# Performance work log

Hardware: AMD Instinct MI355X
Metric: run time of the kernel (lower is better)

## Reference

```python
import jax, jax.numpy as jnp
import numpy as np

B, S, V, D, H, DK, DFF, L = 2, 1024, 513, 512, 8, 64, 2048, 6
PAD_IDX = -1.0
EPS_GPE = 0.1

def _sinusoid_table(n_position, d_hid):
    pos = np.arange(n_position)[:, None].astype(np.float64)
    i = np.arange(d_hid)[None, :]
    angle = pos / np.power(10000.0, 2 * (i // 2) / d_hid)
    tab = np.zeros((n_position, d_hid), dtype=np.float32)
    tab[:, 0::2] = np.sin(angle[:, 0::2])
    tab[:, 1::2] = np.cos(angle[:, 1::2])
    return jnp.asarray(tab)

_POS_TABLE = _sinusoid_table(2048, D)

def _ln(x, g, b, eps=1e-6):
    m = x.mean(-1, keepdims=True)
    v = x.var(-1, keepdims=True)
    return (x - m) * jax.lax.rsqrt(v + eps) * g + b

def _mha(x_q, x_kv, wq_, wk_, wv_, wo_, mask, g, b):
    Bq, Sq, _ = x_q.shape
    Skv = x_kv.shape[1]
    q = (x_q @ wq_).reshape(Bq, Sq, H, DK).transpose(0, 2, 1, 3)
    k = (x_kv @ wk_).reshape(Bq, Skv, H, DK).transpose(0, 2, 1, 3)
    v = (x_kv @ wv_).reshape(Bq, Skv, H, DK).transpose(0, 2, 1, 3)
    scores = jnp.einsum('bhqd,bhkd->bhqk', q, k) / np.float32(np.sqrt(DK))
    scores = jnp.where(mask[:, None], scores, jnp.float32(-1e9))
    attn = jax.nn.softmax(scores, axis=-1)
    out = jnp.einsum('bhqk,bhkd->bhqd', attn, v).transpose(0, 2, 1, 3).reshape(Bq, Sq, D)
    return _ln(x_q + out @ wo_, g, b)

def _forward(dec_in, prev_dec_out, trg, adj, graph_length, gr_mask, gr_pos_enc_kernel,
             emb_w1, emb_b1, emb_w2, emb_b2, emb_w3, emb_b3, ln0_g, ln0_b,
             wq, wk, wv, wo, ln1_g, ln1_b,
             cq, ck, cv, co, ln2_g, ln2_b,
             ffn_w1, ffn_b1, ffn_w2, ffn_b2, ln3_g, ln3_b,
             p_w1, p_b1, p_w2, p_b2, p_w3, p_b3):
    # masks (n_ensemble = 1 so dec_in[:, :, 0, :] == dec_in)
    causal = jnp.tril(jnp.ones((S, S), bool))
    slf_mask = jnp.all(dec_in != PAD_IDX, -1)[:, None, :] & causal          # [B,S,S]
    enc_mask = jnp.all(prev_dec_out != PAD_IDX, -1)[:, None, :]             # [B,1,S]
    # word-embedding MLP: 513 -> 513 -> 513 -> 512
    h = jax.nn.relu(dec_in @ emb_w1 + emb_b1)
    h = jax.nn.relu(h @ emb_w2 + emb_b2)
    h = h @ emb_w3 + emb_b3                                                 # [B,S,D]
    # propagation graph positional encoding (k = 0..2, un-normalized branch)
    w = (1.0 - EPS_GPE) ** jnp.arange(gr_pos_enc_kernel.shape[1], dtype=jnp.float32)
    base = _POS_TABLE[:S]                                                   # [S,D]
    emb = jnp.einsum('k,bkst,td->bsd', w, gr_pos_enc_kernel, base) / w.sum()
    h = _ln(h + emb, ln0_g, ln0_b)
    for i in range(L):
        h = _mha(h, h, wq[i], wk[i], wv[i], wo[i], slf_mask, ln1_g[i], ln1_b[i])
        h = _mha(h, prev_dec_out, cq[i], ck[i], cv[i], co[i], enc_mask, ln2_g[i], ln2_b[i])
        f = jax.nn.relu(h @ ffn_w1[i] + ffn_b1[i]) @ ffn_w2[i] + ffn_b2[i]
        h = _ln(h + f, ln3_g[i], ln3_b[i])
    # projection head: 512 -> 513 -> 513 -> 513
    z = jax.nn.relu(h @ p_w1 + p_b1)
    z = jax.nn.relu(z @ p_w2 + p_b2)
    return z @ p_w3 + p_b3                                                  # [B,S,V]

def setup_inputs():
    key = jax.random.key(0)
    ks = jax.random.split(key, 24)
    def xavier(k, shape):
        lim = np.float32(np.sqrt(6.0 / (shape[-2] + shape[-1])))
        return jax.random.uniform(k, shape, jnp.float32, -lim, lim)
    inp = {}
    inp['dec_in'] = jax.random.uniform(ks[0], (B, S, V), jnp.float32)
    inp['prev_dec_out'] = jax.random.normal(ks[1], (B, S, D), jnp.float32)
    inp['trg'] = jnp.zeros((B, S, V), jnp.float32)
    inp['adj'] = jnp.zeros((B, S, S), jnp.float32)
    inp['graph_length'] = jnp.zeros((B, S, 10), jnp.float32)
    inp['gr_mask'] = jnp.zeros((B, 1, S, S), jnp.float32)
    gk = jax.random.uniform(ks[2], (B, 3, S, S), jnp.float32)
    inp['gr_pos_enc_kernel'] = gk / jnp.sum(gk, -1, keepdims=True)  # row-stochastic diffusion kernels
    SZ = max(V, D)  # sz_intermed = 513
    inp['emb_w1'] = xavier(ks[3], (V, SZ)); inp['emb_b1'] = jnp.zeros((SZ,))
    inp['emb_w2'] = xavier(ks[4], (SZ, SZ)); inp['emb_b2'] = jnp.zeros((SZ,))
    inp['emb_w3'] = xavier(ks[5], (SZ, D)); inp['emb_b3'] = jnp.zeros((D,))
    inp['ln0_g'] = jnp.ones((D,)); inp['ln0_b'] = jnp.zeros((D,))
    for name, ki, shp in [('wq', 6, (L, D, D)), ('wk', 7, (L, D, D)), ('wv', 8, (L, D, D)), ('wo', 9, (L, D, D)),
                          ('cq', 10, (L, D, D)), ('ck', 11, (L, D, D)), ('cv', 12, (L, D, D)), ('co', 13, (L, D, D)),
                          ('ffn_w1', 14, (L, D, DFF)), ('ffn_w2', 15, (L, DFF, D))]:
        inp[name] = xavier(ks[ki], shp)
    inp['ffn_b1'] = jnp.zeros((L, DFF)); inp['ffn_b2'] = jnp.zeros((L, D))
    inp['ln1_g'] = jnp.ones((L, D)); inp['ln1_b'] = jnp.zeros((L, D))
    inp['ln2_g'] = jnp.ones((L, D)); inp['ln2_b'] = jnp.zeros((L, D))
    inp['ln3_g'] = jnp.ones((L, D)); inp['ln3_b'] = jnp.zeros((L, D))
    inp['p_w1'] = xavier(ks[16], (D, V)); inp['p_b1'] = jnp.zeros((V,))
    inp['p_w2'] = xavier(ks[17], (V, V)); inp['p_b2'] = jnp.zeros((V,))
    inp['p_w3'] = xavier(ks[18], (V, V)); inp['p_b3'] = jnp.zeros((V,))
    return inp

def reference(dec_in, prev_dec_out, trg, adj, graph_length, gr_mask, gr_pos_enc_kernel,
              emb_w1, emb_b1, emb_w2, emb_b2, emb_w3, emb_b3, ln0_g, ln0_b,
              wq, wk, wv, wo, ln1_g, ln1_b,
              cq, ck, cv, co, ln2_g, ln2_b,
              ffn_w1, ffn_b1, ffn_w2, ffn_b2, ln3_g, ln3_b,
              p_w1, p_b1, p_w2, p_b2, p_w3, p_b3):
    return _forward(dec_in, prev_dec_out, trg, adj, graph_length, gr_mask, gr_pos_enc_kernel,
                    emb_w1, emb_b1, emb_w2, emb_b2, emb_w3, emb_b3, ln0_g, ln0_b,
                    wq, wk, wv, wo, ln1_g, ln1_b,
                    cq, ck, cv, co, ln2_g, ln2_b,
                    ffn_w1, ffn_b1, ffn_w2, ffn_b2, ln3_g, ln3_b,
                    p_w1, p_b1, p_w2, p_b2, p_w3, p_b3)
```

## Files before the change

kernel.cpp:

```cpp
#include <hip/hip_runtime.h>
#include <hip/hip_bf16.h>
#include <stdint.h>

#define BB 2
#define SS 1024
#define VV 513
#define VP 576
#define DD 512
#define HH 8
#define DKK 64
#define DFFN 2048
#define LL 6
#define MM (BB * SS)

typedef __bf16 bf16x8 __attribute__((ext_vector_type(8)));
typedef float f32x4 __attribute__((ext_vector_type(4)));
typedef unsigned short us8 __attribute__((ext_vector_type(8)));
typedef unsigned short us4 __attribute__((ext_vector_type(4)));

static __device__ inline unsigned short f2bf(float f) {
  union { float f; unsigned u; } v; v.f = f;
  unsigned u = v.u;
  unsigned r = (u + 0x7FFFu + ((u >> 16) & 1u)) >> 16;
  return (unsigned short)r;
}

static __device__ inline bf16x8 ldfrag(const unsigned short* p) {
  us8 r = *(const us8*)p;
  return __builtin_bit_cast(bf16x8, r);
}

typedef __attribute__((address_space(3))) void lds_void;
typedef const __attribute__((address_space(1))) void glb_void;
static __device__ inline void gl_lds16(const void* g, void* l) {
  __builtin_amdgcn_global_load_lds((glb_void*)g, (lds_void*)l, 16, 0, 0);
}

static __device__ inline bf16x8 ldfrag_swz(const unsigned short* base, int row, int kloc) {
  const unsigned byte = (unsigned)(row * 128 + kloc * 2) ^ (unsigned)((row & 7) << 4);
  return ldfrag((const unsigned short*)((const char*)base + byte));
}

static __device__ inline int rot3(int x) { return (x == 2) ? 0 : x + 1; }

struct GemmP {
  const unsigned short* A;
  const unsigned short* B0; const unsigned short* B1; const unsigned short* B2;
  const float* bias;
  float* C;
  unsigned short* D0; unsigned short* D1; unsigned short* D2;
  int Kp, Np, ldc, Nreal, relu;
};

template<int NB, int NT, int TRV, int KS>
__global__ __launch_bounds__(256)
void gemm_tpl(GemmP p)
{
  constexpr int FN = NT / 32;
  __shared__ unsigned short Al[3][64 * 64];
  __shared__ unsigned short Bl[3][NT * 64];
  const int tid = threadIdx.x;
  const int l = tid & 63, w = tid >> 6;
  const int wm = w >> 1, wn = w & 1;
  const int lr = l & 15, lg = l >> 4;

  const int nbn = p.Np / NT;
  int sel = 0, bx = blockIdx.x;
  if (NB > 1) { sel = bx / nbn; bx -= sel * nbn; }
  const unsigned short* Bmat = p.B0;
  if (NB > 1 && sel == 1) Bmat = p.B1;
  if (NB > 2 && sel == 2) Bmat = p.B2;
  const int m0 = blockIdx.y << 6, n0 = bx * NT;
  const int kz = (KS > 1) ? blockIdx.z : 0;

  f32x4 acc[2][FN];
  const f32x4 zf = {0.f, 0.f, 0.f, 0.f};
#pragma unroll
  for (int i = 0; i < 2; ++i)
#pragma unroll
    for (int j = 0; j < FN; ++j) acc[i][j] = zf;

  const size_t Kp = (size_t)p.Kp;
  const unsigned short* Abase = p.A + (size_t)m0 * Kp;
  const unsigned short* Bbase = Bmat + (size_t)n0 * Kp;
  const int nt = (p.Kp >> 6) / KS;
  const int kb0 = kz * nt;

  auto stage = [&](int buf, int kt) {
    const int k0 = (kb0 + kt) << 6;
#pragma unroll
    for (int j = 0; j < 2; ++j) {
      const int ti = j * 256 + tid;
      const int row = ti >> 3;
      const int ch = (ti & 7) ^ (row & 7);
      gl_lds16(Abase + (size_t)row * Kp + k0 + ch * 8, &Al[buf][ti * 8]);
    }
#pragma unroll
    for (int j = 0; j < FN; ++j) {
      const int ti = j * 256 + tid;
      const int row = ti >> 3;
      const int ch = (ti & 7) ^ (row & 7);
      gl_lds16(Bbase + (size_t)row * Kp + k0 + ch * 8, &Bl[buf][ti * 8]);
    }
  };

  stage(0, 0);
  if (nt > 1) stage(1, 1);
  int cb = 0, sb = 2;

  for (int kt = 0; kt < nt; ++kt) {
    if (kt + 1 < nt) {
      if constexpr (FN == 2) asm volatile("s_waitcnt vmcnt(4)" ::: "memory");
      else                   asm volatile("s_waitcnt vmcnt(6)" ::: "memory");
    } else {
      asm volatile("s_waitcnt vmcnt(0)" ::: "memory");
    }
    __builtin_amdgcn_s_barrier();
    if (kt + 2 < nt) { stage(sb, kt + 2); sb = rot3(sb); }
#pragma unroll
    for (int ks = 0; ks < 2; ++ks) {
      bf16x8 af[2], bfv[FN];
#pragma unroll
      for (int mf = 0; mf < 2; ++mf)
        af[mf] = ldfrag_swz(Al[cb], wm * 32 + mf * 16 + lr, ks * 32 + lg * 8);
#pragma unroll
      for (int nf = 0; nf < FN; ++nf)
        bfv[nf] = ldfrag_swz(Bl[cb], wn * (NT / 2) + nf * 16 + lr, ks * 32 + lg * 8);
#pragma unroll
      for (int mf = 0; mf < 2; ++mf)
#pragma unroll
        for (int nf = 0; nf < FN; ++nf)
          acc[mf][nf] = __builtin_amdgcn_mfma_f32_16x16x32_bf16(af[mf], bfv[nf], acc[mf][nf], 0, 0, 0);
    }
    cb = rot3(cb);
  }

  unsigned short* Dsel = p.D0;
  if (NB > 1 && sel == 1) Dsel = p.D1;
  if (NB > 2 && sel == 2) Dsel = p.D2;

  if (TRV && sel == 2) {
#pragma unroll
    for (int mf = 0; mf < 2; ++mf) {
      const int growb = m0 + wm * 32 + mf * 16 + (lg << 2);
      const int b = growb >> 10, s = growb & 1023;
#pragma unroll
      for (int nf = 0; nf < FN; ++nf) {
        const int gcol = n0 + wn * (NT / 2) + nf * 16 + lr;
        const int h = gcol >> 6, d = gcol & 63;
        us4 t;
#pragma unroll
        for (int r = 0; r < 4; ++r) t[r] = f2bf(acc[mf][nf][r]);
        *(us4*)(Dsel + (((size_t)(b * HH) + h) * DKK + d) * SS + s) = t;
      }
    }
    return;
  }

  float* Cz = p.C ? (p.C + (size_t)kz * MM * p.ldc) : nullptr;
#pragma unroll
  for (int mf = 0; mf < 2; ++mf) {
#pragma unroll
    for (int r = 0; r < 4; ++r) {
      const int grow = m0 + wm * 32 + mf * 16 + (lg << 2) + r;
#pragma unroll
      for (int nf = 0; nf < FN; ++nf) {
        const int gcol = n0 + wn * (NT / 2) + nf * 16 + lr;
        float v = acc[mf][nf][r];
        if (p.bias && kz == 0 && gcol < p.Nreal) v += p.bias[gcol];
        if (p.relu) v = fmaxf(v, 0.f);
        if (Dsel) Dsel[(size_t)grow * p.Np + gcol] = f2bf(v);
        if (Cz && gcol < p.Nreal) Cz[(size_t)grow * p.ldc + gcol] = v;
      }
    }
  }
}

struct GemmBat {
  const unsigned short* A;
  const unsigned short* B[12];
  unsigned short* D[12];
  int Kp, Np;
};

__global__ __launch_bounds__(256)
void gemm_bat(GemmBat p)
{
  __shared__ unsigned short Al[3][64 * 64];
  __shared__ unsigned short Bl[3][64 * 64];
  const int tid = threadIdx.x;
  const int l = tid & 63, w = tid >> 6;
  const int wm = w >> 1, wn = w & 1;
  const int lr = l & 15, lg = l >> 4;

  const int nbn = p.Np >> 6;
  const int sel = blockIdx.x / nbn;
  const int bx = blockIdx.x - sel * nbn;
  const unsigned short* Bmat = p.B[sel];
  unsigned short* Dmat = p.D[sel];
  const int m0 = blockIdx.y << 6, n0 = bx << 6;

  f32x4 acc[2][2];
  const f32x4 zf = {0.f, 0.f, 0.f, 0.f};
#pragma unroll
  for (int i = 0; i < 2; ++i)
#pragma unroll
    for (int j = 0; j < 2; ++j) acc[i][j] = zf;

  const size_t Kp = (size_t)p.Kp;
  const unsigned short* Abase = p.A + (size_t)m0 * Kp;
  const unsigned short* Bbase = Bmat + (size_t)n0 * Kp;

  auto stage = [&](int buf, int kt) {
    const int k0 = kt << 6;
#pragma unroll
    for (int j = 0; j < 2; ++j) {
      const int ti = j * 256 + tid;
      const int row = ti >> 3;
      const int ch = (ti & 7) ^ (row & 7);
      gl_lds16(Abase + (size_t)row * Kp + k0 + ch * 8, &Al[buf][ti * 8]);
    }
#pragma unroll
    for (int j = 0; j < 2; ++j) {
      const int ti = j * 256 + tid;
      const int row = ti >> 3;
      const int ch = (ti & 7) ^ (row & 7);
      gl_lds16(Bbase + (size_t)row * Kp + k0 + ch * 8, &Bl[buf][ti * 8]);
    }
  };

  const int nt = p.Kp >> 6;
  stage(0, 0);
  if (nt > 1) stage(1, 1);
  int cb = 0, sb = 2;

  for (int kt = 0; kt < nt; ++kt) {
    if (kt + 1 < nt) asm volatile("s_waitcnt vmcnt(4)" ::: "memory");
    else             asm volatile("s_waitcnt vmcnt(0)" ::: "memory");
    __builtin_amdgcn_s_barrier();
    if (kt + 2 < nt) { stage(sb, kt + 2); sb = rot3(sb); }
#pragma unroll
    for (int ks = 0; ks < 2; ++ks) {
      bf16x8 af[2], bfv[2];
#pragma unroll
      for (int mf = 0; mf < 2; ++mf)
        af[mf] = ldfrag_swz(Al[cb], wm * 32 + mf * 16 + lr, ks * 32 + lg * 8);
#pragma unroll
      for (int nf = 0; nf < 2; ++nf)
        bfv[nf] = ldfrag_swz(Bl[cb], wn * 32 + nf * 16 + lr, ks * 32 + lg * 8);
#pragma unroll
      for (int mf = 0; mf < 2; ++mf)
#pragma unroll
        for (int nf = 0; nf < 2; ++nf)
          acc[mf][nf] = __builtin_amdgcn_mfma_f32_16x16x32_bf16(af[mf], bfv[nf], acc[mf][nf], 0, 0, 0);
    }
    cb = rot3(cb);
  }

  if (sel & 1) {
#pragma unroll
    for (int mf = 0; mf < 2; ++mf) {
      const int growb = m0 + wm * 32 + mf * 16 + (lg << 2);
      const int b = growb >> 10, s = growb & 1023;
#pragma unroll
      for (int nf = 0; nf < 2; ++nf) {
        const int gcol = n0 + wn * 32 + nf * 16 + lr;
        const int h = gcol >> 6, d = gcol & 63;
        us4 t;
#pragma unroll
        for (int r = 0; r < 4; ++r) t[r] = f2bf(acc[mf][nf][r]);
        *(us4*)(Dmat + (((size_t)(b * HH) + h) * DKK + d) * SS + s) = t;
      }
    }
    return;
  }

#pragma unroll
  for (int mf = 0; mf < 2; ++mf) {
#pragma unroll
    for (int r = 0; r < 4; ++r) {
      const int grow = m0 + wm * 32 + mf * 16 + (lg << 2) + r;
#pragma unroll
      for (int nf = 0; nf < 2; ++nf) {
        const int gcol = n0 + wn * 32 + nf * 16 + lr;
        Dmat[(size_t)grow * p.Np + gcol] = f2bf(acc[mf][nf][r]);
      }
    }
  }
}

template<int CAUSAL>
__global__ __launch_bounds__(128)
void attn_kernel(const unsigned short* __restrict__ Qb,
                 const unsigned short* __restrict__ Kb,
                 const unsigned short* __restrict__ VbT,
                 unsigned short* __restrict__ Ob,
                 const float* __restrict__ maskadd)
{
  __shared__ unsigned short Kl[2][2][64 * 64];
  __shared__ unsigned short Vl[2][2][64 * 64];
  __shared__ char PC[9216];
  unsigned short* Pl = (unsigned short*)PC;
  float (*comb)[66] = (float(*)[66])PC;

  const int tid = threadIdx.x;
  const int l = tid & 63, w = tid >> 6;
  const int qt = blockIdx.x, h = blockIdx.y, b = blockIdx.z;
  const int lr = l & 15, lg = l >> 4;

  bf16x8 qf[2][2];
#pragma unroll
  for (int mf = 0; mf < 2; ++mf) {
    const unsigned short* qrow = Qb + ((size_t)(b * SS) + qt * 32 + mf * 16 + lr) * DD + h * DKK;
    qf[mf][0] = ldfrag(qrow + (lg << 3));
    qf[mf][1] = ldfrag(qrow + 32 + (lg << 3));
  }

  const unsigned short* Kbase = Kb + (size_t)(b * SS) * DD + h * DKK;
  const unsigned short* Vbase = VbT + ((size_t)(b * HH) + h) * DKK * SS;

  auto stage = [&](int buf, int kt) {
#pragma unroll
    for (int j = 0; j < 8; ++j) {
      const int ti = j * 64 + l;
      const int row = ti >> 3;
      const int ch = (ti & 7) ^ (row & 7);
      gl_lds16(Kbase + (size_t)(kt * 64 + row) * DD + ch * 8, &Kl[w][buf][ti * 8]);
    }
#pragma unroll
    for (int j = 0; j < 8; ++j) {
      const int ti = j * 64 + l;
      const int row = ti >> 3;
      const int ch = (ti & 7) ^ (row & 7);
      gl_lds16(Vbase + (size_t)row * SS + kt * 64 + ch * 8, &Vl[w][buf][ti * 8]);
    }
  };

  f32x4 accO[2][4];
  const f32x4 zf = {0.f, 0.f, 0.f, 0.f};
#pragma unroll
  for (int mf = 0; mf < 2; ++mf)
#pragma unroll
    for (int nf = 0; nf < 4; ++nf) accO[mf][nf] = zf;
  float mold[2][4], lsum[2][4];
#pragma unroll
  for (int mf = 0; mf < 2; ++mf)
#pragma unroll
    for (int r = 0; r < 4; ++r) { mold[mf][r] = -1e30f; lsum[mf][r] = 0.f; }

  const int ktmax = CAUSAL ? ((qt >> 1) + 1) : (SS / 64);
  const int myn = (ktmax - w + 1) >> 1;

  if (myn > 0) stage(0, w);
  int buf = 0;

  for (int i = 0; i < myn; ++i) {
    const int kt = w + 2 * i;
    if (i + 1 < myn) {
      stage(buf ^ 1, kt + 2);
      asm volatile("s_waitcnt vmcnt(16)" ::: "memory");
    } else {
      asm volatile("s_waitcnt vmcnt(0)" ::: "memory");
    }
    const unsigned short* KB = &Kl[w][buf][0];
    const unsigned short* VB = &Vl[w][buf][0];
    float sc[2][4][4];
    __builtin_amdgcn_s_setprio(1);
#pragma unroll
    for (int nf = 0; nf < 4; ++nf) {
      bf16x8 k0 = ldfrag_swz(KB, nf * 16 + lr, lg * 8);
      bf16x8 k1 = ldfrag_swz(KB, nf * 16 + lr, 32 + lg * 8);
      const int kglob = kt * 64 + nf * 16 + lr;
      const float madd = maskadd[b * SS + kglob];
#pragma unroll
      for (int mf = 0; mf < 2; ++mf) {
        f32x4 s = zf;
        s = __builtin_amdgcn_mfma_f32_16x16x32_bf16(qf[mf][0], k0, s, 0, 0, 0);
        s = __builtin_amdgcn_mfma_f32_16x16x32_bf16(qf[mf][1], k1, s, 0, 0, 0);
#pragma unroll
        for (int r = 0; r < 4; ++r) {
          const int qglob = qt * 32 + mf * 16 + (lg << 2) + r;
          sc[mf][nf][r] = (CAUSAL && kglob > qglob) ? -1e9f : s[r] * 0.125f + madd;
        }
      }
    }
    __builtin_amdgcn_s_setprio(0);
#pragma unroll
    for (int mf = 0; mf < 2; ++mf)
#pragma unroll
      for (int r = 0; r < 4; ++r) {
        float mloc = fmaxf(fmaxf(sc[mf][0][r], sc[mf][1][r]), fmaxf(sc[mf][2][r], sc[mf][3][r]));
#pragma unroll
        for (int off = 1; off < 16; off <<= 1)
          mloc = fmaxf(mloc, __shfl_xor(mloc, off, 64));
        const float mnew = fmaxf(mold[mf][r], mloc);
        const float corr = __expf(mold[mf][r] - mnew);
        float ps = 0.f;
#pragma unroll
        for (int nf = 0; nf < 4; ++nf) {
          const float pv = __expf(sc[mf][nf][r] - mnew);
          sc[mf][nf][r] = pv;
          ps += pv;
        }
#pragma unroll
        for (int off = 1; off < 16; off <<= 1)
          ps += __shfl_xor(ps, off, 64);
        lsum[mf][r] = lsum[mf][r] * corr + ps;
#pragma unroll
        for (int nf = 0; nf < 4; ++nf) accO[mf][nf][r] *= corr;
        mold[mf][r] = mnew;
      }
    unsigned short* pw = Pl + w * 32 * 72;
#pragma unroll
    for (int mf = 0; mf < 2; ++mf)
#pragma unroll
      for (int nf = 0; nf < 4; ++nf)
#pragma unroll
        for (int r = 0; r < 4; ++r)
          pw[(mf * 16 + (lg << 2) + r) * 72 + nf * 16 + lr] = f2bf(sc[mf][nf][r]);
    bf16x8 pa[2][2];
#pragma unroll
    for (int mf = 0; mf < 2; ++mf) {
      pa[mf][0] = ldfrag(&pw[(mf * 16 + lr) * 72 + (lg << 3)]);
      pa[mf][1] = ldfrag(&pw[(mf * 16 + lr) * 72 + 32 + (lg << 3)]);
    }
    __builtin_amdgcn_s_setprio(1);
#pragma unroll
    for (int nf = 0; nf < 4; ++nf) {
      bf16x8 v0 = ldfrag_swz(VB, nf * 16 + lr, lg * 8);
      bf16x8 v1 = ldfrag_swz(VB, nf * 16 + lr, 32 + lg * 8);
#pragma unroll
      for (int mf = 0; mf < 2; ++mf) {
        accO[mf][nf] = __builtin_amdgcn_mfma_f32_16x16x32_bf16(pa[mf][0], v0, accO[mf][nf], 0, 0, 0);
        accO[mf][nf] = __builtin_amdgcn_mfma_f32_16x16x32_bf16(pa[mf][1], v1, accO[mf][nf], 0, 0, 0);
      }
    }
    __builtin_amdgcn_s_setprio(0);
    buf ^= 1;
  }

  __syncthreads();
  if (w == 1) {
#pragma unroll
    for (int mf = 0; mf < 2; ++mf)
#pragma unroll
      for (int r = 0; r < 4; ++r) {
        const int qrow = mf * 16 + (lg << 2) + r;
#pragma unroll
        for (int nf = 0; nf < 4; ++nf)
          comb[qrow][nf * 16 + lr] = accO[mf][nf][r];
        if (lr == 0) { comb[qrow][64] = mold[mf][r]; comb[qrow][65] = lsum[mf][r]; }
      }
  }
  __syncthreads();
  if (w == 0) {
#pragma unroll
    for (int mf = 0; mf < 2; ++mf)
#pragma unroll
      for (int r = 0; r < 4; ++r) {
        const int qrow = mf * 16 + (lg << 2) + r;
        const float m1 = comb[qrow][64], l1 = comb[qrow][65];
        const float m0v = mold[mf][r], l0 = lsum[mf][r];
        const float ms = fmaxf(m0v, m1);
        const float f0 = __expf(m0v - ms), f1 = __expf(m1 - ms);
        const float inv = 1.f / (l0 * f0 + l1 * f1);
        const size_t orow = ((size_t)(b * SS) + qt * 32 + mf * 16 + (lg << 2) + r) * DD + h * DKK;
#pragma unroll
        for (int nf = 0; nf < 4; ++nf)
          Ob[orow + nf * 16 + lr] =
              f2bf((accO[mf][nf][r] * f0 + comb[qrow][nf * 16 + lr] * f1) * inv);
      }
  }
}

template<int P>
__global__ __launch_bounds__(256)
void addln_kernel(const float* __restrict__ a, const float* __restrict__ c,
                  const float* __restrict__ g, const float* __restrict__ bb,
                  float* __restrict__ hf, unsigned short* __restrict__ hb)
{
  const int row = blockIdx.x * 4 + (threadIdx.x >> 6);
  const int l = threadIdx.x & 63;
  const float* ar = a + (size_t)row * DD + l * 8;
  f32x4 x0 = *(const f32x4*)ar;
  f32x4 x1 = *(const f32x4*)(ar + 4);
#pragma unroll
  for (int pp = 0; pp < P; ++pp) {
    const float* cr = c + (size_t)pp * MM * DD + (size_t)row * DD + l * 8;
    x0 += *(const f32x4*)cr;
    x1 += *(const f32x4*)(cr + 4);
  }
  float sum = x0[0] + x0[1] + x0[2] + x0[3] + x1[0] + x1[1] + x1[2] + x1[3];
#pragma unroll
  for (int off = 1; off < 64; off <<= 1) sum += __shfl_xor(sum, off, 64);
  const float mean = sum * (1.f / 512.f);
  float vs = 0.f;
#pragma unroll
  for (int j = 0; j < 4; ++j) { float d0 = x0[j] - mean; float d1 = x1[j] - mean; vs += d0 * d0 + d1 * d1; }
#pragma unroll
  for (int off = 1; off < 64; off <<= 1) vs += __shfl_xor(vs, off, 64);
  const float rs = rsqrtf(vs * (1.f / 512.f) + 1e-6f);
  const f32x4 g0 = *(const f32x4*)(g + l * 8), g1 = *(const f32x4*)(g + l * 8 + 4);
  const f32x4 b0 = *(const f32x4*)(bb + l * 8), b1 = *(const f32x4*)(bb + l * 8 + 4);
  f32x4 o0, o1;
  us8 ob;
#pragma unroll
  for (int j = 0; j < 4; ++j) {
    o0[j] = (x0[j] - mean) * rs * g0[j] + b0[j];
    o1[j] = (x1[j] - mean) * rs * g1[j] + b1[j];
    ob[j] = f2bf(o0[j]); ob[j + 4] = f2bf(o1[j]);
  }
  float* of = hf + (size_t)row * DD + l * 8;
  *(f32x4*)of = o0; *(f32x4*)(of + 4) = o1;
  *(us8*)(hb + (size_t)row * DD + l * 8) = ob;
}

template<int NCOLS, int NPAD>
__global__ __launch_bounds__(64)
void prep_row(const float* __restrict__ x, unsigned short* __restrict__ xb,
              float* __restrict__ mask)
{
  const int row = blockIdx.x, l = threadIdx.x;
  const float* xr = x + (size_t)row * NCOLS;
  unsigned short* ob = xb + (size_t)row * NPAD;
  int ok = 1;
  for (int j = l; j < NPAD; j += 64) {
    if (j < NCOLS) {
      const float v = xr[j];
      ok &= (v != -1.0f) ? 1 : 0;
      ob[j] = f2bf(v);
    } else {
      ob[j] = 0;
    }
  }
  ok = __all(ok) ? 1 : 0;
  if (l == 0) mask[row] = ok ? 0.f : -1e9f;
}

__global__ void postable_kernel(unsigned short* __restrict__ tabT)
{
  const int i = blockIdx.x * blockDim.x + threadIdx.x;
  if (i >= DD * SS) return;
  const int d = i >> 10, s = i & 1023;
  const float ex = (float)(2 * (d >> 1)) * (1.0f / (float)DD);
  const float ang = (float)s * exp2f(ex * -13.287712379549449f);
  tabT[i] = f2bf((d & 1) ? cosf(ang) : sinf(ang));
}

__global__ void gpec_kernel(const float* __restrict__ gk, unsigned short* __restrict__ Mb)
{
  const int i = blockIdx.x * blockDim.x + threadIdx.x;
  if (i >= BB * SS * SS) return;
  const int b = i / (SS * SS);
  const int rem = i - b * (SS * SS);
  const float* p = gk + (size_t)b * 3 * SS * SS + rem;
  Mb[i] = f2bf((p[0] + 0.9f * p[SS * SS] + 0.81f * p[2 * SS * SS]) * (1.0f / 2.71f));
}

__global__ __launch_bounds__(256)
void wconv_kernel(const float* __restrict__ W, unsigned short* __restrict__ WT,
                  int K, int N, int Kp, int Np)
{
  __shared__ float t[64][65];
  const float* Wl = W + (size_t)blockIdx.z * K * N;
  unsigned short* WTl = WT + (size_t)blockIdx.z * Np * Kp;
  const int n0 = blockIdx.x << 6, k0 = blockIdx.y << 6;
  const int tid = threadIdx.x;
  const int cx = tid & 63, ry = tid >> 6;
#pragma unroll
  for (int i = 0; i < 16; ++i) {
    const int kk = k0 + ry + i * 4, nn = n0 + cx;
    t[ry + i * 4][cx] = (kk < K && nn < N) ? Wl[(size_t)kk * N + nn] : 0.f;
  }
  __syncthreads();
#pragma unroll
  for (int i = 0; i < 16; ++i) {
    const int nn = n0 + ry + i * 4, kk = k0 + cx;
    WTl[(size_t)nn * Kp + kk] = f2bf(t[cx][ry + i * 4]);
  }
}

struct WconvB { const float* W[8]; unsigned short* WT[8]; };
__global__ __launch_bounds__(256)
void wconv8_kernel(WconvB p)
{
  __shared__ float t[64][65];
  const int z = blockIdx.z;
  const int wi = z / LL, li = z - wi * LL;
  const float* Wl = p.W[wi] + (size_t)li * DD * DD;
  unsigned short* WTl = p.WT[wi] + (size_t)li * DD * DD;
  const int n0 = blockIdx.x << 6, k0 = blockIdx.y << 6;
  const int cx = threadIdx.x & 63, ry = threadIdx.x >> 6;
#pragma unroll
  for (int i = 0; i < 16; ++i)
    t[ry + i * 4][cx] = Wl[(size_t)(k0 + ry + i * 4) * DD + n0 + cx];
  __syncthreads();
#pragma unroll
  for (int i = 0; i < 16; ++i)
    WTl[(size_t)(n0 + ry + i * 4) * DD + k0 + cx] = f2bf(t[cx][ry + i * 4]);
}

static inline void g1(hipStream_t s, const unsigned short* A, const unsigned short* B,
                      const float* bias, float* C, unsigned short* D,
                      int Kp, int Np, int ldc, int Nreal, int relu)
{
  GemmP p{};
  p.A = A; p.B0 = B; p.bias = bias; p.C = C; p.D0 = D;
  p.Kp = Kp; p.Np = Np; p.ldc = ldc; p.Nreal = Nreal; p.relu = relu;
  gemm_tpl<1, 64, 0, 1><<<dim3(Np >> 6, MM >> 6), 256, 0, s>>>(p);
}

static inline void g1w(hipStream_t s, const unsigned short* A, const unsigned short* B,
                       const float* bias, unsigned short* D, int Kp, int Np, int relu)
{
  GemmP p{};
  p.A = A; p.B0 = B; p.bias = bias; p.D0 = D;
  p.Kp = Kp; p.Np = Np; p.ldc = Np; p.Nreal = Np; p.relu = relu;
  gemm_tpl<1, 128, 0, 1><<<dim3(Np >> 7, MM >> 6), 256, 0, s>>>(p);
}

static inline void g1k4(hipStream_t s, const unsigned short* A, const unsigned short* B,
                        const float* bias, float* C, int Kp)
{
  GemmP p{};
  p.A = A; p.B0 = B; p.bias = bias; p.C = C;
  p.Kp = Kp; p.Np = DD; p.ldc = DD; p.Nreal = DD; p.relu = 0;
  gemm_tpl<1, 64, 0, 4><<<dim3(DD >> 6, MM >> 6, 4), 256, 0, s>>>(p);
}

static inline void g3t(hipStream_t s, const unsigned short* A, const unsigned short* B0,
                       const unsigned short* B1, const unsigned short* B2,
                       unsigned short* D0, unsigned short* D1, unsigned short* D2T)
{
  GemmP p{};
  p.A = A; p.B0 = B0; p.B1 = B1; p.B2 = B2; p.D0 = D0; p.D1 = D1; p.D2 = D2T;
  p.Kp = DD; p.Np = DD; p.ldc = DD; p.Nreal = DD; p.relu = 0;
  gemm_tpl<3, 64, 1, 1><<<dim3(3 * (DD >> 6), MM >> 6), 256, 0, s>>>(p);
}

extern "C" void kernel_launch(void* const* d_in, const int* in_sizes, int n_in,
                              void* d_out, int out_size, void* d_ws, size_t ws_size,
                              hipStream_t stream)
{
  (void)in_sizes; (void)n_in; (void)out_size; (void)ws_size;
  const float* dec_in = (const float*)d_in[0];
  const float* prev   = (const float*)d_in[1];
  const float* gk     = (const float*)d_in[6];
  const float* emb_w1 = (const float*)d_in[7];
  const float* emb_b1 = (const float*)d_in[8];
  const float* emb_w2 = (const float*)d_in[9];
  const float* emb_b2 = (const float*)d_in[10];
  const float* emb_w3 = (const float*)d_in[11];
  const float* emb_b3 = (const float*)d_in[12];
  const float* ln0_g  = (const float*)d_in[13];
  const float* ln0_b  = (const float*)d_in[14];
  const float* wq     = (const float*)d_in[15];
  const float* wk     = (const float*)d_in[16];
  const float* wv     = (const float*)d_in[17];
  const float* wo     = (const float*)d_in[18];
  const float* cq     = (const float*)d_in[19];
  const float* ck     = (const float*)d_in[20];
  const float* cv     = (const float*)d_in[21];
  const float* co     = (const float*)d_in[22];
  const float* ffn_w1 = (const float*)d_in[23];
  const float* ffn_w2 = (const float*)d_in[24];
  const float* ffn_b1 = (const float*)d_in[25];
  const float* ffn_b2 = (const float*)d_in[26];
  const float* ln1_g  = (const float*)d_in[27];
  const float* ln1_b  = (const float*)d_in[28];
  const float* ln2_g  = (const float*)d_in[29];
  const float* ln2_b  = (const float*)d_in[30];
  const float* ln3_g  = (const float*)d_in[31];
  const float* ln3_b  = (const float*)d_in[32];
  const float* p_w1   = (const float*)d_in[33];
  const float* p_b1   = (const float*)d_in[34];
  const float* p_w2   = (const float*)d_in[35];
  const float* p_b2   = (const float*)d_in[36];
  const float* p_w3   = (const float*)d_in[37];
  const float* p_b3   = (const float*)d_in[38];

  char* wsp = (char*)d_ws;
  auto carve = [&](size_t bytes) { char* r = wsp; wsp += (bytes + 255) & ~(size_t)255; return r; };

  unsigned short* decb  = (unsigned short*)carve((size_t)MM * VP * 2);
  unsigned short* prevb = (unsigned short*)carve((size_t)MM * DD * 2);
  float*          hf    = (float*)carve((size_t)MM * DD * 4);
  unsigned short* hb    = (unsigned short*)carve((size_t)MM * DD * 2);
  float*          xf1   = (float*)carve((size_t)MM * DD * 4);
  unsigned short* tb1   = (unsigned short*)carve((size_t)MM * DFFN * 2);
  unsigned short* Mbb   = tb1;
  float*          xf2   = (float*)((char*)tb1 + (size_t)MM * SS * 2);
  unsigned short* tb2a  = (unsigned short*)carve((size_t)MM * VP * 2);
  unsigned short* tb2b  = (unsigned short*)carve((size_t)MM * VP * 2);
  unsigned short* qb    = (unsigned short*)carve((size_t)MM * DD * 2);
  unsigned short* kb    = (unsigned short*)carve((size_t)MM * DD * 2);
  unsigned short* vbT   = (unsigned short*)carve((size_t)MM * DD * 2);
  float* kvs = (float*)carve((size_t)MM * 4);
  float* kve = (float*)carve((size_t)MM * 4);
  unsigned short* postabt = (unsigned short*)carve((size_t)DD * SS * 2);
  unsigned short* ew1t  = (unsigned short*)carve((size_t)VP * VP * 2);
  unsigned short* ew2t  = (unsigned short*)carve((size_t)VP * VP * 2);
  unsigned short* ew3t  = (unsigned short*)carve((size_t)DD * VP * 2);
  unsigned short* wqt   = (unsigned short*)carve((size_t)LL * DD * DD * 2);
  unsigned short* wkt   = (unsigned short*)carve((size_t)LL * DD * DD * 2);
  unsigned short* wvt   = (unsigned short*)carve((size_t)LL * DD * DD * 2);
  unsigned short* wot   = (unsigned short*)carve((size_t)LL * DD * DD * 2);
  unsigned short* cqt   = (unsigned short*)carve((size_t)LL * DD * DD * 2);
  unsigned short* ckt   = (unsigned short*)carve((size_t)LL * DD * DD * 2);
  unsigned short* cvt   = (unsigned short*)carve((size_t)LL * DD * DD * 2);
  unsigned short* cot   = (unsigned short*)carve((size_t)LL * DD * DD * 2);
  unsigned short* f1t   = (unsigned short*)carve((size_t)LL * DFFN * DD * 2);
  unsigned short* f2t   = (unsigned short*)carve((size_t)LL * DD * DFFN * 2);
  unsigned short* p1t   = (unsigned short*)carve((size_t)VP * DD * 2);
  unsigned short* p2t   = (unsigned short*)carve((size_t)VP * VP * 2);
  unsigned short* p3t   = (unsigned short*)carve((size_t)VP * VP * 2);
  unsigned short* ckall = (unsigned short*)carve((size_t)LL * MM * DD * 2);
  unsigned short* cvbT  = (unsigned short*)carve((size_t)LL * MM * DD * 2);
  float*          xk4   = (float*)carve((size_t)4 * MM * DD * 4);

  const dim3 agrid(SS / 32, HH, BB);

  prep_row<VV, VP><<<MM, 64, 0, stream>>>(dec_in, decb, kvs);
  prep_row<DD, DD><<<MM, 64, 0, stream>>>(prev, prevb, kve);
  postable_kernel<<<(DD * SS + 255) / 256, 256, 0, stream>>>(postabt);
  gpec_kernel<<<(BB * SS * SS + 255) / 256, 256, 0, stream>>>(gk, Mbb);

  {
    WconvB wb{};
    wb.W[0] = wq; wb.W[1] = wk; wb.W[2] = wv; wb.W[3] = wo;
    wb.W[4] = cq; wb.W[5] = ck; wb.W[6] = cv; wb.W[7] = co;
    wb.WT[0] = wqt; wb.WT[1] = wkt; wb.WT[2] = wvt; wb.WT[3] = wot;
    wb.WT[4] = cqt; wb.WT[5] = ckt; wb.WT[6] = cvt; wb.WT[7] = cot;
    wconv8_kernel<<<dim3(8, 8, 8 * LL), 256, 0, stream>>>(wb);
  }
  wconv_kernel<<<dim3(9, 9, 1), 256, 0, stream>>>(emb_w1, ew1t, VV, VV, VP, VP);
  wconv_kernel<<<dim3(9, 9, 1), 256, 0, stream>>>(emb_w2, ew2t, VV, VV, VP, VP);
  wconv_kernel<<<dim3(8, 9, 1), 256, 0, stream>>>(emb_w3, ew3t, VV, DD, VP, DD);
  wconv_kernel<<<dim3(32, 8, LL), 256, 0, stream>>>(ffn_w1, f1t, DD, DFFN, DD, DFFN);
  wconv_kernel<<<dim3(8, 32, LL), 256, 0, stream>>>(ffn_w2, f2t, DFFN, DD, DFFN, DD);
  wconv_kernel<<<dim3(9, 8, 1), 256, 0, stream>>>(p_w1, p1t, DD, VV, DD, VP);
  wconv_kernel<<<dim3(9, 9, 1), 256, 0, stream>>>(p_w2, p2t, VV, VV, VP, VP);
  wconv_kernel<<<dim3(9, 9, 1), 256, 0, stream>>>(p_w3, p3t, VV, VV, VP, VP);

  {
    GemmBat p{};
    p.A = prevb; p.Kp = DD; p.Np = DD;
    for (int i = 0; i < LL; ++i) {
      p.B[2 * i]     = ckt + (size_t)i * DD * DD;
      p.B[2 * i + 1] = cvt + (size_t)i * DD * DD;
      p.D[2 * i]     = ckall + (size_t)i * MM * DD;
      p.D[2 * i + 1] = cvbT + (size_t)i * MM * DD;
    }
    gemm_bat<<<dim3(12 * (DD >> 6), MM >> 6), 256, 0, stream>>>(p);
  }

  g1(stream, decb, ew1t, emb_b1, nullptr, tb2a, VP, VP, VP, VV, 1);
  g1(stream, tb2a, ew2t, emb_b2, nullptr, tb2b, VP, VP, VP, VV, 1);
  g1(stream, tb2b, ew3t, emb_b3, xf1, nullptr, VP, DD, DD, DD, 0);
  g1(stream, Mbb, postabt, nullptr, xf2, nullptr, SS, DD, DD, DD, 0);
  addln_kernel<1><<<MM / 4, 256, 0, stream>>>(xf1, xf2, ln0_g, ln0_b, hf, hb);

  for (int i = 0; i < LL; ++i) {
    const size_t od = (size_t)i * DD * DD;
    g3t(stream, hb, wqt + od, wkt + od, wvt + od, qb, kb, vbT);
    attn_kernel<1><<<agrid, 128, 0, stream>>>(qb, kb, vbT, qb, kvs);
    g1(stream, qb, wot + od, nullptr, xf1, nullptr, DD, DD, DD, DD, 0);
    addln_kernel<1><<<MM / 4, 256, 0, stream>>>(hf, xf1, ln1_g + i * DD, ln1_b + i * DD, hf, hb);
    g1(stream, hb, cqt + od, nullptr, nullptr, qb, DD, DD, DD, DD, 0);
    attn_kernel<0><<<agrid, 128, 0, stream>>>(qb, ckall + (size_t)i * MM * DD,
                                              cvbT + (size_t)i * MM * DD, qb, kve);
    g1(stream, qb, cot + od, nullptr, xf1, nullptr, DD, DD, DD, DD, 0);
    addln_kernel<1><<<MM / 4, 256, 0, stream>>>(hf, xf1, ln2_g + i * DD, ln2_b + i * DD, hf, hb);
    g1w(stream, hb, f1t + (size_t)i * DFFN * DD, ffn_b1 + i * DFFN, tb1, DD, DFFN, 1);
    g1k4(stream, tb1, f2t + (size_t)i * DD * DFFN, ffn_b2 + i * DD, xk4, DFFN);
    addln_kernel<4><<<MM / 4, 256, 0, stream>>>(hf, xk4, ln3_g + i * DD, ln3_b + i * DD, hf, hb);
  }

  g1(stream, hb, p1t, p_b1, nullptr, tb2a, DD, VP, VP, VV, 1);
  g1(stream, tb2a, p2t, p_b2, nullptr, tb2b, VP, VP, VP, VV, 1);
  g1(stream, tb2b, p3t, p_b3, (float*)d_out, nullptr, VP, VP, VV, VV, 0);
}
```

Baseline: 1.071 ms.

## Fuse cross-attention Q projection into attention kernel and merge setup kernels

Adds an attnx kernel that computes the cross-attention query projection (hb × cq slice per head) in-block before running flash attention over the encoder keys. This removes the separate Q GEMM launch and the round trip of Q through global memory. The output projections now use a 2-way split-K GEMM whose partial sums are reduced inside addln. The startup prep kernels are merged into one launch, and the weight conversion kernels into another, to cut launch overhead. The price is redundant Q-projection work, since each head block re-reads the hb rows, plus extra partial-sum traffic in addln.

```diff
diff --git a/kernel.cpp b/kernel.cpp
--- a/kernel.cpp
+++ b/kernel.cpp
@@ -289,7 +289,6 @@
   }
 }
 
-template<int CAUSAL>
 __global__ __launch_bounds__(128)
 void attn_kernel(const unsigned short* __restrict__ Qb,
                  const unsigned short* __restrict__ Kb,
@@ -348,7 +347,7 @@
 #pragma unroll
     for (int r = 0; r < 4; ++r) { mold[mf][r] = -1e30f; lsum[mf][r] = 0.f; }
 
-  const int ktmax = CAUSAL ? ((qt >> 1) + 1) : (SS / 64);
+  const int ktmax = (qt >> 1) + 1;
   const int myn = (ktmax - w + 1) >> 1;
 
   if (myn > 0) stage(0, w);
@@ -380,7 +379,7 @@
 #pragma unroll
         for (int r = 0; r < 4; ++r) {
           const int qglob = qt * 32 + mf * 16 + (lg << 2) + r;
-          sc[mf][nf][r] = (CAUSAL && kglob > qglob) ? -1e9f : s[r] * 0.125f + madd;
+          sc[mf][nf][r] = (kglob > qglob) ? -1e9f : s[r] * 0.125f + madd;
         }
       }
     }
@@ -473,6 +472,253 @@
   }
 }
 
+__global__ __launch_bounds__(128)
+void attnx_kernel(const unsigned short* __restrict__ Hb,
+                  const unsigned short* __restrict__ Wq,
+                  const unsigned short* __restrict__ Kb,
+                  const unsigned short* __restrict__ VbT,
+                  unsigned short* __restrict__ Ob,
+                  const float* __restrict__ maskadd)
+{
+  __shared__ unsigned short Kl[2][2][64 * 64];
+  __shared__ unsigned short Vl[2][2][64 * 64];
+  __shared__ char PC[9216];
+  unsigned short* Pl = (unsigned short*)PC;
+  float (*comb)[66] = (float(*)[66])PC;
+  unsigned short* QA = &Kl[0][0][0];
+  unsigned short* QB = &Vl[0][0][0];
+  unsigned short* Ql = (unsigned short*)PC;
+
+  const int tid = threadIdx.x;
+  const int l = tid & 63, w = tid >> 6;
+  const int qt = blockIdx.x, h = blockIdx.y, b = blockIdx.z;
+  const int lr = l & 15, lg = l >> 4;
+
+  {
+    const unsigned short* Abase = Hb + ((size_t)(b * SS) + qt * 32) * DD;
+    const unsigned short* Bbase = Wq + (size_t)(h * DKK) * DD;
+    auto stage_q = [&](int buf, int kt) {
+      const int k0 = kt << 6;
+#pragma unroll
+      for (int j = 0; j < 2; ++j) {
+        const int ti = j * 128 + tid;
+        const int row = ti >> 3;
+        const int ch = (ti & 7) ^ (row & 7);
+        gl_lds16(Abase + (size_t)row * DD + k0 + ch * 8, &QA[buf * 2048 + ti * 8]);
+      }
+#pragma unroll
+      for (int j = 0; j < 4; ++j) {
+        const int ti = j * 128 + tid;
+        const int row = ti >> 3;
+        const int ch = (ti & 7) ^ (row & 7);
+        gl_lds16(Bbase + (size_t)row * DD + k0 + ch * 8, &QB[buf * 4096 + ti * 8]);
+      }
+    };
+    f32x4 qacc[2][2];
+    const f32x4 zf = {0.f, 0.f, 0.f, 0.f};
+#pragma unroll
+    for (int i = 0; i < 2; ++i)
+#pragma unroll
+      for (int j = 0; j < 2; ++j) qacc[i][j] = zf;
+
+    stage_q(0, 0);
+    for (int kt = 0; kt < 8; ++kt) {
+      if (kt + 1 < 8) {
+        stage_q((kt + 1) & 1, kt + 1);
+        asm volatile("s_waitcnt vmcnt(6)" ::: "memory");
+      } else {
+        asm volatile("s_waitcnt vmcnt(0)" ::: "memory");
+      }
+      __builtin_amdgcn_s_barrier();
+      const unsigned short* qa = &QA[(kt & 1) * 2048];
+      const unsigned short* qbuf = &QB[(kt & 1) * 4096];
+#pragma unroll
+      for (int ks = 0; ks < 2; ++ks) {
+        bf16x8 af[2], bfv[2];
+#pragma unroll
+        for (int mf = 0; mf < 2; ++mf)
+          af[mf] = ldfrag_swz(qa, mf * 16 + lr, ks * 32 + lg * 8);
+#pragma unroll
+        for (int nf = 0; nf < 2; ++nf)
+          bfv[nf] = ldfrag_swz(qbuf, w * 32 + nf * 16 + lr, ks * 32 + lg * 8);
+#pragma unroll
+        for (int mf = 0; mf < 2; ++mf)
+#pragma unroll
+          for (int nf = 0; nf < 2; ++nf)
+            qacc[mf][nf] = __builtin_amdgcn_mfma_f32_16x16x32_bf16(af[mf], bfv[nf], qacc[mf][nf], 0, 0, 0);
+      }
+      __builtin_amdgcn_s_barrier();
+    }
+#pragma unroll
+    for (int mf = 0; mf < 2; ++mf)
+#pragma unroll
+      for (int nf = 0; nf < 2; ++nf)
+#pragma unroll
+        for (int r = 0; r < 4; ++r)
+          Ql[(mf * 16 + (lg << 2) + r) * 72 + w * 32 + nf * 16 + lr] = f2bf(qacc[mf][nf][r] * 0.125f);
+    __syncthreads();
+  }
+  bf16x8 qf[2][2];
+#pragma unroll
+  for (int mf = 0; mf < 2; ++mf) {
+    qf[mf][0] = ldfrag(&Ql[(mf * 16 + lr) * 72 + (lg << 3)]);
+    qf[mf][1] = ldfrag(&Ql[(mf * 16 + lr) * 72 + 32 + (lg << 3)]);
+  }
+  __syncthreads();
+
+  const unsigned short* Kbase = Kb + (size_t)(b * SS) * DD + h * DKK;
+  const unsigned short* Vbase = VbT + ((size_t)(b * HH) + h) * DKK * SS;
+
+  auto stage = [&](int buf, int kt) {
+#pragma unroll
+    for (int j = 0; j < 8; ++j) {
+      const int ti = j * 64 + l;
+      const int row = ti >> 3;
+      const int ch = (ti & 7) ^ (row & 7);
+      gl_lds16(Kbase + (size_t)(kt * 64 + row) * DD + ch * 8, &Kl[w][buf][ti * 8]);
+    }
+#pragma unroll
+    for (int j = 0; j < 8; ++j) {
+      const int ti = j * 64 + l;
+      const int row = ti >> 3;
+      const int ch = (ti & 7) ^ (row & 7);
+      gl_lds16(Vbase + (size_t)row * SS + kt * 64 + ch * 8, &Vl[w][buf][ti * 8]);
+    }
+  };
+
+  f32x4 accO[2][4];
+  const f32x4 zf = {0.f, 0.f, 0.f, 0.f};
+#pragma unroll
+  for (int mf = 0; mf < 2; ++mf)
+#pragma unroll
+    for (int nf = 0; nf < 4; ++nf) accO[mf][nf] = zf;
+  float mold[2][4], lsum[2][4];
+#pragma unroll
+  for (int mf = 0; mf < 2; ++mf)
+#pragma unroll
+    for (int r = 0; r < 4; ++r) { mold[mf][r] = -1e30f; lsum[mf][r] = 0.f; }
+
+  const int myn = (SS / 64 - w + 1) >> 1;
+  stage(0, w);
+  int buf = 0;
+
+  for (int i = 0; i < myn; ++i) {
+    const int kt = w + 2 * i;
+    if (i + 1 < myn) {
+      stage(buf ^ 1, kt + 2);
+      asm volatile("s_waitcnt vmcnt(16)" ::: "memory");
+    } else {
+      asm volatile("s_waitcnt vmcnt(0)" ::: "memory");
+    }
+    const unsigned short* KB = &Kl[w][buf][0];
+    const unsigned short* VB = &Vl[w][buf][0];
+    float sc[2][4][4];
+    __builtin_amdgcn_s_setprio(1);
+#pragma unroll
+    for (int nf = 0; nf < 4; ++nf) {
+      bf16x8 k0 = ldfrag_swz(KB, nf * 16 + lr, lg * 8);
+      bf16x8 k1 = ldfrag_swz(KB, nf * 16 + lr, 32 + lg * 8);
+      const int kglob = kt * 64 + nf * 16 + lr;
+      const float madd = maskadd[b * SS + kglob];
+#pragma unroll
+      for (int mf = 0; mf < 2; ++mf) {
+        f32x4 s = zf;
+        s = __builtin_amdgcn_mfma_f32_16x16x32_bf16(qf[mf][0], k0, s, 0, 0, 0);
+        s = __builtin_amdgcn_mfma_f32_16x16x32_bf16(qf[mf][1], k1, s, 0, 0, 0);
+#pragma unroll
+        for (int r = 0; r < 4; ++r)
+          sc[mf][nf][r] = s[r] + madd;
+      }
+    }
+    __builtin_amdgcn_s_setprio(0);
+#pragma unroll
+    for (int mf = 0; mf < 2; ++mf)
+#pragma unroll
+      for (int r = 0; r < 4; ++r) {
+        float mloc = fmaxf(fmaxf(sc[mf][0][r], sc[mf][1][r]), fmaxf(sc[mf][2][r], sc[mf][3][r]));
+#pragma unroll
+        for (int off = 1; off < 16; off <<= 1)
+          mloc = fmaxf(mloc, __shfl_xor(mloc, off, 64));
+        const float mnew = fmaxf(mold[mf][r], mloc);
+        const float corr = __expf(mold[mf][r] - mnew);
+        float ps = 0.f;
+#pragma unroll
+        for (int nf = 0; nf < 4; ++nf) {
+          const float pv = __expf(sc[mf][nf][r] - mnew);
+          sc[mf][nf][r] = pv;
+          ps += pv;
+        }
+#pragma unroll
+        for (int off = 1; off < 16; off <<= 1)
+          ps += __shfl_xor(ps, off, 64);
+        lsum[mf][r] = lsum[mf][r] * corr + ps;
+#pragma unroll
+        for (int nf = 0; nf < 4; ++nf) accO[mf][nf][r] *= corr;
+        mold[mf][r] = mnew;
+      }
+    unsigned short* pw = Pl + w * 32 * 72;
+#pragma unroll
+    for (int mf = 0; mf < 2; ++mf)
+#pragma unroll
+      for (int nf = 0; nf < 4; ++nf)
+#pragma unroll
+        for (int r = 0; r < 4; ++r)
+          pw[(mf * 16 + (lg << 2) + r) * 72 + nf * 16 + lr] = f2bf(sc[mf][nf][r]);
+    bf16x8 pa[2][2];
+#pragma unroll
+    for (int mf = 0; mf < 2; ++mf) {
+      pa[mf][0] = ldfrag(&pw[(mf * 16 + lr) * 72 + (lg << 3)]);
+      pa[mf][1] = ldfrag(&pw[(mf * 16 + lr) * 72 + 32 + (lg << 3)]);
+    }
+    __builtin_amdgcn_s_setprio(1);
+#pragma unroll
+    for (int nf = 0; nf < 4; ++nf) {
+      bf16x8 v0 = ldfrag_swz(VB, nf * 16 + lr, lg * 8);
+      bf16x8 v1 = ldfrag_swz(VB, nf * 16 + lr, 32 + lg * 8);
+#pragma unroll
+      for (int mf = 0; mf < 2; ++mf) {
+        accO[mf][nf] = __builtin_amdgcn_mfma_f32_16x16x32_bf16(pa[mf][0], v0, accO[mf][nf], 0, 0, 0);
+        accO[mf][nf] = __builtin_amdgcn_mfma_f32_16x16x32_bf16(pa[mf][1], v1, accO[mf][nf], 0, 0, 0);
+      }
+    }
+    __builtin_amdgcn_s_setprio(0);
+    buf ^= 1;
+  }
+
+  __syncthreads();
+  if (w == 1) {
+#pragma unroll
+    for (int mf = 0; mf < 2; ++mf)
+#pragma unroll
+      for (int r = 0; r < 4; ++r) {
+        const int qrow = mf * 16 + (lg << 2) + r;
+#pragma unroll
+        for (int nf = 0; nf < 4; ++nf)
+          comb[qrow][nf * 16 + lr] = accO[mf][nf][r];
+        if (lr == 0) { comb[qrow][64] = mold[mf][r]; comb[qrow][65] = lsum[mf][r]; }
+      }
+  }
+  __syncthreads();
+  if (w == 0) {
+#pragma unroll
+    for (int mf = 0; mf < 2; ++mf)
+#pragma unroll
+      for (int r = 0; r < 4; ++r) {
+        const int qrow = mf * 16 + (lg << 2) + r;
+        const float m1 = comb[qrow][64], l1 = comb[qrow][65];
+        const float m0v = mold[mf][r], l0 = lsum[mf][r];
+        const float ms = fmaxf(m0v, m1);
+        const float f0 = __expf(m0v - ms), f1 = __expf(m1 - ms);
+        const float inv = 1.f / (l0 * f0 + l1 * f1);
+        const size_t orow = ((size_t)(b * SS) + qt * 32 + mf * 16 + (lg << 2) + r) * DD + h * DKK;
+#pragma unroll
+        for (int nf = 0; nf < 4; ++nf)
+          Ob[orow + nf * 16 + lr] =
+              f2bf((accO[mf][nf][r] * f0 + comb[qrow][nf * 16 + lr] * f1) * inv);
+      }
+  }
+}
+
 template<int P>
 __global__ __launch_bounds__(256)
 void addln_kernel(const float* __restrict__ a, const float* __restrict__ c,
@@ -515,58 +761,70 @@
   *(us8*)(hb + (size_t)row * DD + l * 8) = ob;
 }
 
-template<int NCOLS, int NPAD>
-__global__ __launch_bounds__(64)
-void prep_row(const float* __restrict__ x, unsigned short* __restrict__ xb,
-              float* __restrict__ mask)
-{
-  const int row = blockIdx.x, l = threadIdx.x;
-  const float* xr = x + (size_t)row * NCOLS;
-  unsigned short* ob = xb + (size_t)row * NPAD;
-  int ok = 1;
-  for (int j = l; j < NPAD; j += 64) {
-    if (j < NCOLS) {
-      const float v = xr[j];
-      ok &= (v != -1.0f) ? 1 : 0;
-      ob[j] = f2bf(v);
-    } else {
-      ob[j] = 0;
-    }
-  }
-  ok = __all(ok) ? 1 : 0;
-  if (l == 0) mask[row] = ok ? 0.f : -1e9f;
-}
-
-__global__ void postable_kernel(unsigned short* __restrict__ tabT)
-{
-  const int i = blockIdx.x * blockDim.x + threadIdx.x;
-  if (i >= DD * SS) return;
-  const int d = i >> 10, s = i & 1023;
-  const float ex = (float)(2 * (d >> 1)) * (1.0f / (float)DD);
-  const float ang = (float)s * exp2f(ex * -13.287712379549449f);
-  tabT[i] = f2bf((d & 1) ? cosf(ang) : sinf(ang));
-}
-
-__global__ void gpec_kernel(const float* __restrict__ gk, unsigned short* __restrict__ Mb)
-{
-  const int i = blockIdx.x * blockDim.x + threadIdx.x;
-  if (i >= BB * SS * SS) return;
-  const int b = i / (SS * SS);
-  const int rem = i - b * (SS * SS);
-  const float* p = gk + (size_t)b * 3 * SS * SS + rem;
-  Mb[i] = f2bf((p[0] + 0.9f * p[SS * SS] + 0.81f * p[2 * SS * SS]) * (1.0f / 2.71f));
-}
-
 __global__ __launch_bounds__(256)
-void wconv_kernel(const float* __restrict__ W, unsigned short* __restrict__ WT,
-                  int K, int N, int Kp, int Np)
+void prep_all(const float* __restrict__ dec_in, const float* __restrict__ prev,
+              unsigned short* __restrict__ decb, unsigned short* __restrict__ prevb,
+              float* __restrict__ kvs, float* __restrict__ kve,
+              unsigned short* __restrict__ tabT,
+              const float* __restrict__ gk, unsigned short* __restrict__ Mb)
+{
+  const int blk = blockIdx.x, tid = threadIdx.x;
+  if (blk < 1024) {
+    const int isdec = blk < 512;
+    const int row = (isdec ? blk : blk - 512) * 4 + (tid >> 6);
+    const int l = tid & 63;
+    const int NC = isdec ? VV : DD, NP = isdec ? VP : DD;
+    const float* xr = (isdec ? dec_in : prev) + (size_t)row * NC;
+    unsigned short* ob = (isdec ? decb : prevb) + (size_t)row * NP;
+    int ok = 1;
+    for (int j = l; j < NP; j += 64) {
+      if (j < NC) {
+        const float v = xr[j];
+        ok &= (v != -1.0f) ? 1 : 0;
+        ob[j] = f2bf(v);
+      } else ob[j] = 0;
+    }
+    ok = __all(ok) ? 1 : 0;
+    if (l == 0) (isdec ? kvs : kve)[row] = ok ? 0.f : -1e9f;
+  } else if (blk < 3072) {
+    const int i = (blk - 1024) * 256 + tid;
+    const int d = i >> 10, s = i & 1023;
+    const float ex = (float)(2 * (d >> 1)) * (1.0f / (float)DD);
+    const float ang = (float)s * exp2f(ex * -13.287712379549449f);
+    tabT[i] = f2bf((d & 1) ? cosf(ang) : sinf(ang));
+  } else {
+    const int i = (blk - 3072) * 256 + tid;
+    const int b = i / (SS * SS);
+    const int rem = i - b * (SS * SS);
+    const float* p = gk + (size_t)b * 3 * SS * SS + rem;
+    Mb[i] = f2bf((p[0] + 0.9f * p[SS * SS] + 0.81f * p[2 * SS * SS]) * (1.0f / 2.71f));
+  }
+}
+
+struct WJobs {
+  const float* W[8]; unsigned short* WT[8];
+  int K[8], N[8], Kp[8], Np[8], nbx[8], nby[8];
+  int off[9];
+};
+__global__ __launch_bounds__(256)
+void wconv_all(WJobs p)
 {
   __shared__ float t[64][65];
-  const float* Wl = W + (size_t)blockIdx.z * K * N;
-  unsigned short* WTl = WT + (size_t)blockIdx.z * Np * Kp;
-  const int n0 = blockIdx.x << 6, k0 = blockIdx.y << 6;
-  const int tid = threadIdx.x;
-  const int cx = tid & 63, ry = tid >> 6;
+  const int bid = blockIdx.x;
+  int j = 0;
+#pragma unroll
+  for (int i = 0; i < 8; ++i) if (bid >= p.off[i + 1]) j = i + 1;
+  const int local = bid - p.off[j];
+  const int per = p.nbx[j] * p.nby[j];
+  const int z = local / per;
+  const int rem = local - z * per;
+  const int by = rem / p.nbx[j];
+  const int bx = rem - by * p.nbx[j];
+  const int K = p.K[j], N = p.N[j], Kp = p.Kp[j], Np = p.Np[j];
+  const float* Wl = p.W[j] + (size_t)z * K * N;
+  unsigned short* WTl = p.WT[j] + (size_t)z * Np * Kp;
+  const int n0 = bx << 6, k0 = by << 6;
+  const int cx = threadIdx.x & 63, ry = threadIdx.x >> 6;
 #pragma unroll
   for (int i = 0; i < 16; ++i) {
     const int kk = k0 + ry + i * 4, nn = n0 + cx;
@@ -576,7 +834,7 @@
 #pragma unroll
   for (int i = 0; i < 16; ++i) {
     const int nn = n0 + ry + i * 4, kk = k0 + cx;
-    WTl[(size_t)nn * Kp + kk] = f2bf(t[cx][ry + i * 4]);
+    if (nn < Np && kk < Kp) WTl[(size_t)nn * Kp + kk] = f2bf(t[cx][ry + i * 4]);
   }
 }
 
@@ -619,13 +877,14 @@
   gemm_tpl<1, 128, 0, 1><<<dim3(Np >> 7, MM >> 6), 256, 0, s>>>(p);
 }
 
-static inline void g1k4(hipStream_t s, const unsigned short* A, const unsigned short* B,
-                        const float* bias, float* C, int Kp)
+template<int KS>
+static inline void g1k(hipStream_t s, const unsigned short* A, const unsigned short* B,
+                       const float* bias, float* C, int Kp)
 {
   GemmP p{};
   p.A = A; p.B0 = B; p.bias = bias; p.C = C;
   p.Kp = Kp; p.Np = DD; p.ldc = DD; p.Nreal = DD; p.relu = 0;
-  gemm_tpl<1, 64, 0, 4><<<dim3(DD >> 6, MM >> 6, 4), 256, 0, s>>>(p);
+  gemm_tpl<1, 64, 0, KS><<<dim3(DD >> 6, MM >> 6, KS), 256, 0, s>>>(p);
 }
 
 static inline void g3t(hipStream_t s, const unsigned short* A, const unsigned short* B0,
@@ -720,10 +979,7 @@
 
   const dim3 agrid(SS / 32, HH, BB);
 
-  prep_row<VV, VP><<<MM, 64, 0, stream>>>(dec_in, decb, kvs);
-  prep_row<DD, DD><<<MM, 64, 0, stream>>>(prev, prevb, kve);
-  postable_kernel<<<(DD * SS + 255) / 256, 256, 0, stream>>>(postabt);
-  gpec_kernel<<<(BB * SS * SS + 255) / 256, 256, 0, stream>>>(gk, Mbb);
+  prep_all<<<11264, 256, 0, stream>>>(dec_in, prev, decb, prevb, kvs, kve, postabt, gk, Mbb);
 
   {
     WconvB wb{};
@@ -733,14 +989,26 @@
     wb.WT[4] = cqt; wb.WT[5] = ckt; wb.WT[6] = cvt; wb.WT[7] = cot;
     wconv8_kernel<<<dim3(8, 8, 8 * LL), 256, 0, stream>>>(wb);
   }
-  wconv_kernel<<<dim3(9, 9, 1), 256, 0, stream>>>(emb_w1, ew1t, VV, VV, VP, VP);
-  wconv_kernel<<<dim3(9, 9, 1), 256, 0, stream>>>(emb_w2, ew2t, VV, VV, VP, VP);
-  wconv_kernel<<<dim3(8, 9, 1), 256, 0, stream>>>(emb_w3, ew3t, VV, DD, VP, DD);
-  wconv_kernel<<<dim3(32, 8, LL), 256, 0, stream>>>(ffn_w1, f1t, DD, DFFN, DD, DFFN);
-  wconv_kernel<<<dim3(8, 32, LL), 256, 0, stream>>>(ffn_w2, f2t, DFFN, DD, DFFN, DD);
-  wconv_kernel<<<dim3(9, 8, 1), 256, 0, stream>>>(p_w1, p1t, DD, VV, DD, VP);
-  wconv_kernel<<<dim3(9, 9, 1), 256, 0, stream>>>(p_w2, p2t, VV, VV, VP, VP);
-  wconv_kernel<<<dim3(9, 9, 1), 256, 0, stream>>>(p_w3, p3t, VV, VV, VP, VP);
+  {
+    WJobs wj{};
+    const float* Ws[8]   = {emb_w1, emb_w2, emb_w3, ffn_w1, ffn_w2, p_w1, p_w2, p_w3};
+    unsigned short* Ds[8] = {ew1t, ew2t, ew3t, f1t, f2t, p1t, p2t, p3t};
+    const int Ks[8]  = {VV, VV, VV, DD, DFFN, DD, VV, VV};
+    const int Ns[8]  = {VV, VV, DD, DFFN, DD, VV, VV, VV};
+    const int Kps[8] = {VP, VP, VP, DD, DFFN, DD, VP, VP};
+    const int Nps[8] = {VP, VP, DD, DFFN, DD, VP, VP, VP};
+    const int nls[8] = {1, 1, 1, LL, LL, 1, 1, 1};
+    int off = 0;
+    for (int j = 0; j < 8; ++j) {
+      wj.W[j] = Ws[j]; wj.WT[j] = Ds[j];
+      wj.K[j] = Ks[j]; wj.N[j] = Ns[j]; wj.Kp[j] = Kps[j]; wj.Np[j] = Nps[j];
+      wj.nbx[j] = (Nps[j] + 63) / 64; wj.nby[j] = (Kps[j] + 63) / 64;
+      wj.off[j] = off;
+      off += wj.nbx[j] * wj.nby[j] * nls[j];
+    }
+    wj.off[8] = off;
+    wconv_all<<<off, 256, 0, stream>>>(wj);
+  }
 
   {
     GemmBat p{};
@@ -763,16 +1031,15 @@
   for (int i = 0; i < LL; ++i) {
     const size_t od = (size_t)i * DD * DD;
     g3t(stream, hb, wqt + od, wkt + od, wvt + od, qb, kb, vbT);
-    attn_kernel<1><<<agrid, 128, 0, stream>>>(qb, kb, vbT, qb, kvs);
-    g1(stream, qb, wot + od, nullptr, xf1, nullptr, DD, DD, DD, DD, 0);
-    addln_kernel<1><<<MM / 4, 256, 0, stream>>>(hf, xf1, ln1_g + i * DD, ln1_b + i * DD, hf, hb);
-    g1(stream, hb, cqt + od, nullptr, nullptr, qb, DD, DD, DD, DD, 0);
-    attn_kernel<0><<<agrid, 128, 0, stream>>>(qb, ckall + (size_t)i * MM * DD,
-                                              cvbT + (size_t)i * MM * DD, qb, kve);
-    g1(stream, qb, cot + od, nullptr, xf1, nullptr, DD, DD, DD, DD, 0);
-    addln_kernel<1><<<MM / 4, 256, 0, stream>>>(hf, xf1, ln2_g + i * DD, ln2_b + i * DD, hf, hb);
+    attn_kernel<<<agrid, 128, 0, stream>>>(qb, kb, vbT, qb, kvs);
+    g1k<2>(stream, qb, wot + od, nullptr, xk4, DD);
+    addln_kernel<2><<<MM / 4, 256, 0, stream>>>(hf, xk4, ln1_g + i * DD, ln1_b + i * DD, hf, hb);
+    attnx_kernel<<<agrid, 128, 0, stream>>>(hb, cqt + od, ckall + (size_t)i * MM * DD,
+                                            cvbT + (size_t)i * MM * DD, qb, kve);
+    g1k<2>(stream, qb, cot + od, nullptr, xk4, DD);
+    addln_kernel<2><<<MM / 4, 256, 0, stream>>>(hf, xk4, ln2_g + i * DD, ln2_b + i * DD, hf, hb);
     g1w(stream, hb, f1t + (size_t)i * DFFN * DD, ffn_b1 + i * DFFN, tb1, DD, DFFN, 1);
-    g1k4(stream, tb1, f2t + (size_t)i * DD * DFFN, ffn_b2 + i * DD, xk4, DFFN);
+    g1k<4>(stream, tb1, f2t + (size_t)i * DD * DFFN, ffn_b2 + i * DD, xk4, DFFN);
     addln_kernel<4><<<MM / 4, 256, 0, stream>>>(hf, xk4, ln3_g + i * DD, ln3_b + i * DD, hf, hb);
   }
 
```

After: 994.0 us (median of 2 runs). 7.2% less time.
